# Optimization experiments

Hardware: AMD Instinct MI355X
Metric: run time of the kernel (lower is better)

The kernel has to match this reference:

```python
import jax, jax.numpy as jnp
import numpy as np

B, S, D, H = 4, 2048, 1024, 16
HD = D // H


def setup_inputs() -> dict:
    key = jax.random.key(0)
    ks = jax.random.split(key, 5)
    s_in = 1.0 / np.sqrt(D)
    return {
        "x": jax.random.normal(ks[0], (B, S, D), dtype=jnp.float32),
        "W_attn": jax.random.uniform(ks[1], (D, 3 * D), dtype=jnp.float32, minval=-s_in, maxval=s_in),
        "b_attn": jax.random.uniform(ks[2], (3 * D,), dtype=jnp.float32, minval=-s_in, maxval=s_in),
        "W_proj": jax.random.uniform(ks[3], (D, D), dtype=jnp.float32, minval=-s_in, maxval=s_in),
        "b_proj": jax.random.uniform(ks[4], (D,), dtype=jnp.float32, minval=-s_in, maxval=s_in),
    }


def reference(x, W_attn, b_attn, W_proj, b_proj):
    b, s, d = x.shape
    qkv = x @ W_attn + b_attn                      # [B,S,3D]
    q, k, v = jnp.split(qkv, 3, axis=-1)
    # [B,H,S,HD]
    q = q.reshape(b, s, H, HD).transpose(0, 2, 1, 3)
    k = k.reshape(b, s, H, HD).transpose(0, 2, 1, 3)
    v = v.reshape(b, s, H, HD).transpose(0, 2, 1, 3)
    scale = 1.0 / np.sqrt(HD)
    att = jnp.einsum("bhqd,bhkd->bhqk", q, k) * scale
    causal = jnp.tril(jnp.ones((s, s), dtype=bool))
    att = jnp.where(causal[None, None], att, -jnp.inf)
    att = jax.nn.softmax(att, axis=-1)
    y = jnp.einsum("bhqk,bhkd->bhqd", att, v)      # [B,H,S,HD]
    y = y.transpose(0, 2, 1, 3).reshape(b, s, d)
    return y @ W_proj + b_proj
```

## Files before the change

### kernel.cpp

```cpp
#include <hip/hip_runtime.h>

#define B_  4
#define S_  2048
#define D_  1024
#define H_  16
#define HD_ 64
#define BS_ (B_*S_)

typedef _Float16 f16;
typedef _Float16 f16_8 __attribute__((ext_vector_type(8)));
typedef float    f32_4 __attribute__((ext_vector_type(4)));
typedef unsigned int u32;

#define MFMA16(a,b,c) __builtin_amdgcn_mfma_f32_16x16x32_f16(a, b, c, 0, 0, 0)
#define NEG_INF (-__builtin_inff())

__device__ inline void gl_lds16(const f16* g, f16* lds_base, int chunk_base) {
    __builtin_amdgcn_global_load_lds(
        (const __attribute__((address_space(1))) u32*)g,
        (__attribute__((address_space(3))) u32*)(lds_base + (size_t)chunk_base * 8),
        16, 0, 0);
}

__global__ __launch_bounds__(256) void trans_w(
    const float* __restrict__ W, f16* __restrict__ Wt, int ncols)
{
    __shared__ f16 T[64][72];
    const int t = threadIdx.x;
    const int n0 = blockIdx.x * 64, k0 = blockIdx.y * 64;
    const int nl4 = (t & 15) * 4;
    #pragma unroll
    for (int r = 0; r < 4; r++) {
        const int kl = (t >> 4) + r * 16;
        float4 v = *(const float4*)&W[(size_t)(k0 + kl) * ncols + n0 + nl4];
        T[nl4 + 0][kl] = (f16)v.x;
        T[nl4 + 1][kl] = (f16)v.y;
        T[nl4 + 2][kl] = (f16)v.z;
        T[nl4 + 3][kl] = (f16)v.w;
    }
    __syncthreads();
    const int nr = t >> 2, kc = (t & 3) * 16;
    *(uint4*)&Wt[(size_t)(n0 + nr) * 1024 + k0 + kc]     = *(uint4*)&T[nr][kc];
    *(uint4*)&Wt[(size_t)(n0 + nr) * 1024 + k0 + kc + 8] = *(uint4*)&T[nr][kc + 8];
}

__global__ __launch_bounds__(256) void qkv_gemm(
    const float* __restrict__ X,
    const f16*   __restrict__ Wta,
    const float* __restrict__ bias,
    f16* __restrict__ Qb, f16* __restrict__ Kb, f16* __restrict__ Vt)
{
    __shared__ f16 lds[17408];
    f16* Af = lds;
    f16* Bs = lds + 128*40;
    f16* Ct = lds;

    const int t    = threadIdx.x;
    const int lane = t & 63;
    const int w    = t >> 6;
    const int quad = lane >> 4, l15 = lane & 15;
    const int wr = w >> 1, wc = w & 1;
    const int n0 = blockIdx.x * 128;
    const int m0 = blockIdx.y * 128;

    f32_4 acc[4][4] = {};
    const int am = t >> 1, ak = (t & 1) * 16;
    const int wbase = t & 192;

    for (int k0 = 0; k0 < 1024; k0 += 32) {
        #pragma unroll
        for (int c = 0; c < 2; c++) {
            int i = c*256 + t;
            gl_lds16(Wta + (size_t)(n0 + (i >> 2)) * 1024 + k0 + (i & 3) * 8,
                     Bs, c*256 + wbase);
        }
        {
            const float* xs = X + (size_t)(m0 + am) * 1024 + k0 + ak;
            float4 a0 = *(const float4*)(xs);
            float4 a1 = *(const float4*)(xs + 4);
            float4 a2 = *(const float4*)(xs + 8);
            float4 a3 = *(const float4*)(xs + 12);
            f16 hb[16] = {(f16)a0.x,(f16)a0.y,(f16)a0.z,(f16)a0.w,
                          (f16)a1.x,(f16)a1.y,(f16)a1.z,(f16)a1.w,
                          (f16)a2.x,(f16)a2.y,(f16)a2.z,(f16)a2.w,
                          (f16)a3.x,(f16)a3.y,(f16)a3.z,(f16)a3.w};
            *(uint4*)&Af[am*40 + ak]     = *(uint4*)&hb[0];
            *(uint4*)&Af[am*40 + ak + 8] = *(uint4*)&hb[8];
        }
        __syncthreads();

        f16_8 af[4], bf[4];
        #pragma unroll
        for (int mi = 0; mi < 4; mi++)
            af[mi] = *(const f16_8*)&Af[(wr*64 + mi*16 + l15)*40 + quad*8];
        #pragma unroll
        for (int ni = 0; ni < 4; ni++)
            bf[ni] = *(const f16_8*)&Bs[(wc*64 + ni*16 + l15)*32 + quad*8];
        #pragma unroll
        for (int mi = 0; mi < 4; mi++)
            #pragma unroll
            for (int ni = 0; ni < 4; ni++)
                acc[mi][ni] = MFMA16(af[mi], bf[ni], acc[mi][ni]);
        __syncthreads();
    }

    const int which = n0 >> 10;
    float bcol[4];
    #pragma unroll
    for (int ni = 0; ni < 4; ni++)
        bcol[ni] = bias[n0 + wc*64 + ni*16 + l15];

    if (which < 2) {
        f16* dst = (which == 0) ? Qb : Kb;
        const float sc = (which == 0) ? 0.125f * 1.44269504f : 1.0f;
        #pragma unroll
        for (int mi = 0; mi < 4; mi++)
        #pragma unroll
        for (int ni = 0; ni < 4; ni++)
        #pragma unroll
        for (int r = 0; r < 4; r++) {
            int m = m0 + wr*64 + mi*16 + quad*4 + r;
            int n = (n0 & 1023) + wc*64 + ni*16 + l15;
            int h = n >> 6, hd = n & 63;
            int b = m >> 11, s = m & 2047;
            dst[((size_t)(b*16 + h)*2048 + s)*64 + hd] =
                (f16)((acc[mi][ni][r] + bcol[ni]) * sc);
        }
    } else {
        #pragma unroll
        for (int mi = 0; mi < 4; mi++)
        #pragma unroll
        for (int ni = 0; ni < 4; ni++)
        #pragma unroll
        for (int r = 0; r < 4; r++) {
            int nl = wc*64 + ni*16 + l15;
            int ml = wr*64 + mi*16 + quad*4 + r;
            Ct[nl*136 + ml] = (f16)(acc[mi][ni][r] + bcol[ni]);
        }
        __syncthreads();
        const int row = t >> 1, sc4 = (t & 1) * 64;
        const int n = (n0 & 1023) + row;
        const int h = n >> 6, hd = n & 63;
        const int b = m0 >> 11, s0 = (m0 & 2047) + sc4;
        f16* dst = Vt + ((size_t)(b*16 + h)*64 + hd)*2048 + s0;
        #pragma unroll
        for (int j = 0; j < 8; j++)
            *(uint4*)&dst[j*8] = *(uint4*)&Ct[row*136 + sc4 + j*8];
    }
}

__global__ __launch_bounds__(256) void attn(
    const f16* __restrict__ Qb,
    const f16* __restrict__ Kb,
    const f16* __restrict__ Vt,
    f16* __restrict__ Y)
{
    __shared__ f16 Ks[64*72];
    __shared__ f16 Vs[64*72];
    __shared__ f16 Pl[4][32*72];

    const int t    = threadIdx.x;
    const int w    = t >> 6;
    const int lane = t & 63;
    const int quad = lane >> 4, l15 = lane & 15;
    const int bh   = blockIdx.y;
    const int b    = bh >> 4, h = bh & 15;

    const f16* qh = Qb + (size_t)bh * S_ * 64;
    const f16* kh = Kb + (size_t)bh * S_ * 64;
    const f16* vt = Vt + (size_t)bh * 64 * S_;

    const int sk = t >> 2, sc = (t & 3) * 8;
    const f16_8 ones = {(f16)1,(f16)1,(f16)1,(f16)1,(f16)1,(f16)1,(f16)1,(f16)1};

    #pragma unroll 1
    for (int sp = 0; sp < 2; sp++) {
        const int qb = sp ? 15 - (int)blockIdx.x : (int)blockIdx.x;
        const int qw = qb*128 + w*32;

        f16_8 qa[2][2];
        #pragma unroll
        for (int rt = 0; rt < 2; rt++)
            #pragma unroll
            for (int c = 0; c < 2; c++)
                qa[rt][c] = *(const f16_8*)&qh[(size_t)(qw + rt*16 + l15)*64 + c*32 + quad*8];

        f32_4 o[2][4] = {};
        f32_4 lacc[2] = {};
        const int ntiles = 2*qb + 2;

        for (int kt = 0; kt < ntiles; kt++) {
            const int kbase = kt * 64;
            *(uint4*)&Ks[sk*72 + sc]      = *(const uint4*)&kh[(size_t)(kbase + sk)*64 + sc];
            *(uint4*)&Ks[sk*72 + sc + 32] = *(const uint4*)&kh[(size_t)(kbase + sk)*64 + sc + 32];
            *(uint4*)&Vs[sk*72 + sc]      = *(const uint4*)&vt[(size_t)sk*2048 + kbase + sc];
            *(uint4*)&Vs[sk*72 + sc + 32] = *(const uint4*)&vt[(size_t)sk*2048 + kbase + sc + 32];
            __syncthreads();

            if (kbase <= qw + 31) {
                f16_8 kb[4][2];
                #pragma unroll
                for (int sub = 0; sub < 4; sub++)
                    #pragma unroll
                    for (int c = 0; c < 2; c++)
                        kb[sub][c] = *(const f16_8*)&Ks[(sub*16 + l15)*72 + c*32 + quad*8];
                f32_4 s[2][4];
                #pragma unroll
                for (int rt = 0; rt < 2; rt++)
                    #pragma unroll
                    for (int sub = 0; sub < 4; sub++) {
                        f32_4 a = {};
                        a = MFMA16(qa[rt][0], kb[sub][0], a);
                        a = MFMA16(qa[rt][1], kb[sub][1], a);
                        s[rt][sub] = a;
                    }

                const bool masked = (kbase + 63 > qw);
                #pragma unroll
                for (int rt = 0; rt < 2; rt++)
                #pragma unroll
                for (int r = 0; r < 4; r++) {
                    float v0 = s[rt][0][r], v1 = s[rt][1][r];
                    float v2 = s[rt][2][r], v3 = s[rt][3][r];
                    if (masked) {
                        const int row = qw + rt*16 + quad*4 + r;
                        v0 = (kbase      + l15 <= row) ? v0 : NEG_INF;
                        v1 = (kbase + 16 + l15 <= row) ? v1 : NEG_INF;
                        v2 = (kbase + 32 + l15 <= row) ? v2 : NEG_INF;
                        v3 = (kbase + 48 + l15 <= row) ? v3 : NEG_INF;
                    }
                    const int prow = (rt*16 + quad*4 + r)*72;
                    Pl[w][prow +      l15] = (f16)__builtin_amdgcn_exp2f(v0);
                    Pl[w][prow + 16 + l15] = (f16)__builtin_amdgcn_exp2f(v1);
                    Pl[w][prow + 32 + l15] = (f16)__builtin_amdgcn_exp2f(v2);
                    Pl[w][prow + 48 + l15] = (f16)__builtin_amdgcn_exp2f(v3);
                }
                asm volatile("s_waitcnt lgkmcnt(0)" ::: "memory");

                f16_8 vb[4][2];
                #pragma unroll
                for (int tt = 0; tt < 4; tt++)
                    #pragma unroll
                    for (int c = 0; c < 2; c++)
                        vb[tt][c] = *(const f16_8*)&Vs[(tt*16 + l15)*72 + c*32 + quad*8];
                #pragma unroll
                for (int rt = 0; rt < 2; rt++) {
                    f16_8 pa0 = *(const f16_8*)&Pl[w][(rt*16 + l15)*72 +      quad*8];
                    f16_8 pa1 = *(const f16_8*)&Pl[w][(rt*16 + l15)*72 + 32 + quad*8];
                    lacc[rt] = MFMA16(pa0, ones, lacc[rt]);
                    lacc[rt] = MFMA16(pa1, ones, lacc[rt]);
                    #pragma unroll
                    for (int tt = 0; tt < 4; tt++) {
                        o[rt][tt] = MFMA16(pa0, vb[tt][0], o[rt][tt]);
                        o[rt][tt] = MFMA16(pa1, vb[tt][1], o[rt][tt]);
                    }
                }
            }
            __syncthreads();
        }

        #pragma unroll
        for (int rt = 0; rt < 2; rt++)
        #pragma unroll
        for (int r = 0; r < 4; r++) {
            float inv = 1.0f / lacc[rt][r];
            int srow = qw + rt*16 + quad*4 + r;
            #pragma unroll
            for (int tt = 0; tt < 4; tt++)
                Y[(size_t)(b*S_ + srow)*1024 + h*64 + tt*16 + l15] =
                    (f16)(o[rt][tt][r] * inv);
        }
    }
}

__global__ __launch_bounds__(256) void proj_gemm(
    const f16* __restrict__ Yb,
    const f16* __restrict__ Wtp,
    const float* __restrict__ bias,
    float* __restrict__ Out)
{
    __shared__ f16 lds2[128*32*2];
    f16* Af = lds2;
    f16* Bs = lds2 + 128*32;

    const int t    = threadIdx.x;
    const int lane = t & 63;
    const int w    = t >> 6;
    const int quad = lane >> 4, l15 = lane & 15;
    const int wr = w >> 1, wc = w & 1;
    const int n0 = blockIdx.x * 128;
    const int m0 = blockIdx.y * 128;
    const int wbase = t & 192;

    f32_4 acc[4][4] = {};

    for (int k0 = 0; k0 < 1024; k0 += 32) {
        #pragma unroll
        for (int c = 0; c < 2; c++) {
            int i = c*256 + t;
            gl_lds16(Yb  + (size_t)(m0 + (i >> 2)) * 1024 + k0 + (i & 3) * 8, Af, c*256 + wbase);
            gl_lds16(Wtp + (size_t)(n0 + (i >> 2)) * 1024 + k0 + (i & 3) * 8, Bs, c*256 + wbase);
        }
        __syncthreads();
        f16_8 af[4], bf[4];
        #pragma unroll
        for (int mi = 0; mi < 4; mi++)
            af[mi] = *(const f16_8*)&Af[(wr*64 + mi*16 + l15)*32 + quad*8];
        #pragma unroll
        for (int ni = 0; ni < 4; ni++)
            bf[ni] = *(const f16_8*)&Bs[(wc*64 + ni*16 + l15)*32 + quad*8];
        #pragma unroll
        for (int mi = 0; mi < 4; mi++)
            #pragma unroll
            for (int ni = 0; ni < 4; ni++)
                acc[mi][ni] = MFMA16(af[mi], bf[ni], acc[mi][ni]);
        __syncthreads();
    }

    #pragma unroll
    for (int mi = 0; mi < 4; mi++)
    #pragma unroll
    for (int ni = 0; ni < 4; ni++)
    #pragma unroll
    for (int r = 0; r < 4; r++) {
        int m = m0 + wr*64 + mi*16 + quad*4 + r;
        int n = n0 + wc*64 + ni*16 + l15;
        Out[(size_t)m*1024 + n] = acc[mi][ni][r] + bias[n];
    }
}

extern "C" void kernel_launch(void* const* d_in, const int* in_sizes, int n_in,
                              void* d_out, int out_size, void* d_ws, size_t ws_size,
                              hipStream_t stream) {
    const float* x      = (const float*)d_in[0];
    const float* W_attn = (const float*)d_in[1];
    const float* b_attn = (const float*)d_in[2];
    const float* W_proj = (const float*)d_in[3];
    const float* b_proj = (const float*)d_in[4];
    float* out = (float*)d_out;

    const size_t per = (size_t)B_ * H_ * S_ * HD_;
    f16* Yb  = (f16*)d_ws;
    f16* Wta = Yb;
    f16* Qb  = Yb + per;
    f16* Kb  = Qb + per;
    f16* Vt  = Kb + per;
    f16* Wtp = Qb;

    trans_w  <<<dim3(48, 16), 256, 0, stream>>>(W_attn, Wta, 3*D_);
    qkv_gemm <<<dim3(24, 64), 256, 0, stream>>>(x, Wta, b_attn, Qb, Kb, Vt);
    attn     <<<dim3(8, 64),  256, 0, stream>>>(Qb, Kb, Vt, Yb);
    trans_w  <<<dim3(16, 16), 256, 0, stream>>>(W_proj, Wtp, D_);
    proj_gemm<<<dim3(8, 64),  256, 0, stream>>>(Yb, Wtp, b_proj, out);
}
```

Measured before the change: 301.1 us.

## Keep attention probabilities in registers, pre-convert X to fp16, widen GEMM K-step

Attention now computes S transposed (K as the A operand), so each lane's exp'd scores already form the A fragment of a 16x16x16 MFMA for the PV product. This removes the per-wave LDS round trip for P and its waitcnt. A separate x2h kernel converts X to fp16 in the output buffer, which lets qkv_gemm load A with direct global-to-LDS loads. Both GEMMs stage 64 K per barrier pair instead of 32. In exchange there is an extra kernel launch and an extra pass over X, and the PV product uses smaller MFMAs (twice as many instructions).

```diff
diff --git a/kernel.cpp b/kernel.cpp
--- a/kernel.cpp
+++ b/kernel.cpp
@@ -9,10 +9,12 @@
 
 typedef _Float16 f16;
 typedef _Float16 f16_8 __attribute__((ext_vector_type(8)));
+typedef _Float16 f16_4 __attribute__((ext_vector_type(4)));
 typedef float    f32_4 __attribute__((ext_vector_type(4)));
 typedef unsigned int u32;
 
-#define MFMA16(a,b,c) __builtin_amdgcn_mfma_f32_16x16x32_f16(a, b, c, 0, 0, 0)
+#define MFMA32(a,b,c) __builtin_amdgcn_mfma_f32_16x16x32_f16(a, b, c, 0, 0, 0)
+#define MFMA16(a,b,c) __builtin_amdgcn_mfma_f32_16x16x16f16(a, b, c, 0, 0, 0)
 #define NEG_INF (-__builtin_inff())
 
 __device__ inline void gl_lds16(const f16* g, f16* lds_base, int chunk_base) {
@@ -20,6 +22,17 @@
         (const __attribute__((address_space(1))) u32*)g,
         (__attribute__((address_space(3))) u32*)(lds_base + (size_t)chunk_base * 8),
         16, 0, 0);
+}
+
+__global__ __launch_bounds__(256) void x2h(
+    const float* __restrict__ X, f16* __restrict__ Xh)
+{
+    const size_t i = ((size_t)blockIdx.x * 256 + threadIdx.x) * 8;
+    float4 a = *(const float4*)&X[i];
+    float4 b = *(const float4*)&X[i + 4];
+    f16 h[8] = {(f16)a.x,(f16)a.y,(f16)a.z,(f16)a.w,
+                (f16)b.x,(f16)b.y,(f16)b.z,(f16)b.w};
+    *(uint4*)&Xh[i] = *(const uint4*)h;
 }
 
 __global__ __launch_bounds__(256) void trans_w(
@@ -45,243 +58,15 @@
 }
 
 __global__ __launch_bounds__(256) void qkv_gemm(
-    const float* __restrict__ X,
+    const f16*   __restrict__ Xh,
     const f16*   __restrict__ Wta,
     const float* __restrict__ bias,
     f16* __restrict__ Qb, f16* __restrict__ Kb, f16* __restrict__ Vt)
 {
     __shared__ f16 lds[17408];
-    f16* Af = lds;
-    f16* Bs = lds + 128*40;
-    f16* Ct = lds;
-
-    const int t    = threadIdx.x;
-    const int lane = t & 63;
-    const int w    = t >> 6;
-    const int quad = lane >> 4, l15 = lane & 15;
-    const int wr = w >> 1, wc = w & 1;
-    const int n0 = blockIdx.x * 128;
-    const int m0 = blockIdx.y * 128;
-
-    f32_4 acc[4][4] = {};
-    const int am = t >> 1, ak = (t & 1) * 16;
-    const int wbase = t & 192;
-
-    for (int k0 = 0; k0 < 1024; k0 += 32) {
-        #pragma unroll
-        for (int c = 0; c < 2; c++) {
-            int i = c*256 + t;
-            gl_lds16(Wta + (size_t)(n0 + (i >> 2)) * 1024 + k0 + (i & 3) * 8,
-                     Bs, c*256 + wbase);
-        }
-        {
-            const float* xs = X + (size_t)(m0 + am) * 1024 + k0 + ak;
-            float4 a0 = *(const float4*)(xs);
-            float4 a1 = *(const float4*)(xs + 4);
-            float4 a2 = *(const float4*)(xs + 8);
-            float4 a3 = *(const float4*)(xs + 12);
-            f16 hb[16] = {(f16)a0.x,(f16)a0.y,(f16)a0.z,(f16)a0.w,
-                          (f16)a1.x,(f16)a1.y,(f16)a1.z,(f16)a1.w,
-                          (f16)a2.x,(f16)a2.y,(f16)a2.z,(f16)a2.w,
-                          (f16)a3.x,(f16)a3.y,(f16)a3.z,(f16)a3.w};
-            *(uint4*)&Af[am*40 + ak]     = *(uint4*)&hb[0];
-            *(uint4*)&Af[am*40 + ak + 8] = *(uint4*)&hb[8];
-        }
-        __syncthreads();
-
-        f16_8 af[4], bf[4];
-        #pragma unroll
-        for (int mi = 0; mi < 4; mi++)
-            af[mi] = *(const f16_8*)&Af[(wr*64 + mi*16 + l15)*40 + quad*8];
-        #pragma unroll
-        for (int ni = 0; ni < 4; ni++)
-            bf[ni] = *(const f16_8*)&Bs[(wc*64 + ni*16 + l15)*32 + quad*8];
-        #pragma unroll
-        for (int mi = 0; mi < 4; mi++)
-            #pragma unroll
-            for (int ni = 0; ni < 4; ni++)
-                acc[mi][ni] = MFMA16(af[mi], bf[ni], acc[mi][ni]);
-        __syncthreads();
-    }
-
-    const int which = n0 >> 10;
-    float bcol[4];
-    #pragma unroll
-    for (int ni = 0; ni < 4; ni++)
-        bcol[ni] = bias[n0 + wc*64 + ni*16 + l15];
-
-    if (which < 2) {
-        f16* dst = (which == 0) ? Qb : Kb;
-        const float sc = (which == 0) ? 0.125f * 1.44269504f : 1.0f;
-        #pragma unroll
-        for (int mi = 0; mi < 4; mi++)
-        #pragma unroll
-        for (int ni = 0; ni < 4; ni++)
-        #pragma unroll
-        for (int r = 0; r < 4; r++) {
-            int m = m0 + wr*64 + mi*16 + quad*4 + r;
-            int n = (n0 & 1023) + wc*64 + ni*16 + l15;
-            int h = n >> 6, hd = n & 63;
-            int b = m >> 11, s = m & 2047;
-            dst[((size_t)(b*16 + h)*2048 + s)*64 + hd] =
-                (f16)((acc[mi][ni][r] + bcol[ni]) * sc);
-        }
-    } else {
-        #pragma unroll
-        for (int mi = 0; mi < 4; mi++)
-        #pragma unroll
-        for (int ni = 0; ni < 4; ni++)
-        #pragma unroll
-        for (int r = 0; r < 4; r++) {
-            int nl = wc*64 + ni*16 + l15;
-            int ml = wr*64 + mi*16 + quad*4 + r;
-            Ct[nl*136 + ml] = (f16)(acc[mi][ni][r] + bcol[ni]);
-        }
-        __syncthreads();
-        const int row = t >> 1, sc4 = (t & 1) * 64;
-        const int n = (n0 & 1023) + row;
-        const int h = n >> 6, hd = n & 63;
-        const int b = m0 >> 11, s0 = (m0 & 2047) + sc4;
-        f16* dst = Vt + ((size_t)(b*16 + h)*64 + hd)*2048 + s0;
-        #pragma unroll
-        for (int j = 0; j < 8; j++)
-            *(uint4*)&dst[j*8] = *(uint4*)&Ct[row*136 + sc4 + j*8];
-    }
-}
-
-__global__ __launch_bounds__(256) void attn(
-    const f16* __restrict__ Qb,
-    const f16* __restrict__ Kb,
-    const f16* __restrict__ Vt,
-    f16* __restrict__ Y)
-{
-    __shared__ f16 Ks[64*72];
-    __shared__ f16 Vs[64*72];
-    __shared__ f16 Pl[4][32*72];
-
-    const int t    = threadIdx.x;
-    const int w    = t >> 6;
-    const int lane = t & 63;
-    const int quad = lane >> 4, l15 = lane & 15;
-    const int bh   = blockIdx.y;
-    const int b    = bh >> 4, h = bh & 15;
-
-    const f16* qh = Qb + (size_t)bh * S_ * 64;
-    const f16* kh = Kb + (size_t)bh * S_ * 64;
-    const f16* vt = Vt + (size_t)bh * 64 * S_;
-
-    const int sk = t >> 2, sc = (t & 3) * 8;
-    const f16_8 ones = {(f16)1,(f16)1,(f16)1,(f16)1,(f16)1,(f16)1,(f16)1,(f16)1};
-
-    #pragma unroll 1
-    for (int sp = 0; sp < 2; sp++) {
-        const int qb = sp ? 15 - (int)blockIdx.x : (int)blockIdx.x;
-        const int qw = qb*128 + w*32;
-
-        f16_8 qa[2][2];
-        #pragma unroll
-        for (int rt = 0; rt < 2; rt++)
-            #pragma unroll
-            for (int c = 0; c < 2; c++)
-                qa[rt][c] = *(const f16_8*)&qh[(size_t)(qw + rt*16 + l15)*64 + c*32 + quad*8];
-
-        f32_4 o[2][4] = {};
-        f32_4 lacc[2] = {};
-        const int ntiles = 2*qb + 2;
-
-        for (int kt = 0; kt < ntiles; kt++) {
-            const int kbase = kt * 64;
-            *(uint4*)&Ks[sk*72 + sc]      = *(const uint4*)&kh[(size_t)(kbase + sk)*64 + sc];
-            *(uint4*)&Ks[sk*72 + sc + 32] = *(const uint4*)&kh[(size_t)(kbase + sk)*64 + sc + 32];
-            *(uint4*)&Vs[sk*72 + sc]      = *(const uint4*)&vt[(size_t)sk*2048 + kbase + sc];
-            *(uint4*)&Vs[sk*72 + sc + 32] = *(const uint4*)&vt[(size_t)sk*2048 + kbase + sc + 32];
-            __syncthreads();
-
-            if (kbase <= qw + 31) {
-                f16_8 kb[4][2];
-                #pragma unroll
-                for (int sub = 0; sub < 4; sub++)
-                    #pragma unroll
-                    for (int c = 0; c < 2; c++)
-                        kb[sub][c] = *(const f16_8*)&Ks[(sub*16 + l15)*72 + c*32 + quad*8];
-                f32_4 s[2][4];
-                #pragma unroll
-                for (int rt = 0; rt < 2; rt++)
-                    #pragma unroll
-                    for (int sub = 0; sub < 4; sub++) {
-                        f32_4 a = {};
-                        a = MFMA16(qa[rt][0], kb[sub][0], a);
-                        a = MFMA16(qa[rt][1], kb[sub][1], a);
-                        s[rt][sub] = a;
-                    }
-
-                const bool masked = (kbase + 63 > qw);
-                #pragma unroll
-                for (int rt = 0; rt < 2; rt++)
-                #pragma unroll
-                for (int r = 0; r < 4; r++) {
-                    float v0 = s[rt][0][r], v1 = s[rt][1][r];
-                    float v2 = s[rt][2][r], v3 = s[rt][3][r];
-                    if (masked) {
-                        const int row = qw + rt*16 + quad*4 + r;
-                        v0 = (kbase      + l15 <= row) ? v0 : NEG_INF;
-                        v1 = (kbase + 16 + l15 <= row) ? v1 : NEG_INF;
-                        v2 = (kbase + 32 + l15 <= row) ? v2 : NEG_INF;
-                        v3 = (kbase + 48 + l15 <= row) ? v3 : NEG_INF;
-                    }
-                    const int prow = (rt*16 + quad*4 + r)*72;
-                    Pl[w][prow +      l15] = (f16)__builtin_amdgcn_exp2f(v0);
-                    Pl[w][prow + 16 + l15] = (f16)__builtin_amdgcn_exp2f(v1);
-                    Pl[w][prow + 32 + l15] = (f16)__builtin_amdgcn_exp2f(v2);
-                    Pl[w][prow + 48 + l15] = (f16)__builtin_amdgcn_exp2f(v3);
-                }
-                asm volatile("s_waitcnt lgkmcnt(0)" ::: "memory");
-
-                f16_8 vb[4][2];
-                #pragma unroll
-                for (int tt = 0; tt < 4; tt++)
-                    #pragma unroll
-                    for (int c = 0; c < 2; c++)
-                        vb[tt][c] = *(const f16_8*)&Vs[(tt*16 + l15)*72 + c*32 + quad*8];
-                #pragma unroll
-                for (int rt = 0; rt < 2; rt++) {
-                    f16_8 pa0 = *(const f16_8*)&Pl[w][(rt*16 + l15)*72 +      quad*8];
-                    f16_8 pa1 = *(const f16_8*)&Pl[w][(rt*16 + l15)*72 + 32 + quad*8];
-                    lacc[rt] = MFMA16(pa0, ones, lacc[rt]);
-                    lacc[rt] = MFMA16(pa1, ones, lacc[rt]);
-                    #pragma unroll
-                    for (int tt = 0; tt < 4; tt++) {
-                        o[rt][tt] = MFMA16(pa0, vb[tt][0], o[rt][tt]);
-                        o[rt][tt] = MFMA16(pa1, vb[tt][1], o[rt][tt]);
-                    }
-                }
-            }
-            __syncthreads();
-        }
-
-        #pragma unroll
-        for (int rt = 0; rt < 2; rt++)
-        #pragma unroll
-        for (int r = 0; r < 4; r++) {
-            float inv = 1.0f / lacc[rt][r];
-            int srow = qw + rt*16 + quad*4 + r;
-            #pragma unroll
-            for (int tt = 0; tt < 4; tt++)
-                Y[(size_t)(b*S_ + srow)*1024 + h*64 + tt*16 + l15] =
-                    (f16)(o[rt][tt][r] * inv);
-        }
-    }
-}
-
-__global__ __launch_bounds__(256) void proj_gemm(
-    const f16* __restrict__ Yb,
-    const f16* __restrict__ Wtp,
-    const float* __restrict__ bias,
-    float* __restrict__ Out)
-{
-    __shared__ f16 lds2[128*32*2];
-    f16* Af = lds2;
-    f16* Bs = lds2 + 128*32;
+    f16* Af[2] = {lds,        lds + 4096};
+    f16* Bf[2] = {lds + 8192, lds + 12288};
+    f16* Ct    = lds;
 
     const int t    = threadIdx.x;
     const int lane = t & 63;
@@ -294,26 +79,249 @@
 
     f32_4 acc[4][4] = {};
 
-    for (int k0 = 0; k0 < 1024; k0 += 32) {
-        #pragma unroll
-        for (int c = 0; c < 2; c++) {
-            int i = c*256 + t;
-            gl_lds16(Yb  + (size_t)(m0 + (i >> 2)) * 1024 + k0 + (i & 3) * 8, Af, c*256 + wbase);
-            gl_lds16(Wtp + (size_t)(n0 + (i >> 2)) * 1024 + k0 + (i & 3) * 8, Bs, c*256 + wbase);
-        }
-        __syncthreads();
-        f16_8 af[4], bf[4];
+    for (int k0 = 0; k0 < 1024; k0 += 64) {
+        #pragma unroll
+        for (int kc = 0; kc < 2; kc++)
+            #pragma unroll
+            for (int c = 0; c < 2; c++) {
+                int i = c*256 + t;
+                const int row = i >> 2, col = (i & 3) * 8;
+                gl_lds16(Xh  + (size_t)(m0 + row)*1024 + k0 + kc*32 + col,
+                         Af[kc], c*256 + wbase);
+                gl_lds16(Wta + (size_t)(n0 + row)*1024 + k0 + kc*32 + col,
+                         Bf[kc], c*256 + wbase);
+            }
+        __syncthreads();
+
+        #pragma unroll
+        for (int kc = 0; kc < 2; kc++) {
+            f16_8 af[4], bf[4];
+            #pragma unroll
+            for (int mi = 0; mi < 4; mi++)
+                af[mi] = *(const f16_8*)&Af[kc][(wr*64 + mi*16 + l15)*32 + quad*8];
+            #pragma unroll
+            for (int ni = 0; ni < 4; ni++)
+                bf[ni] = *(const f16_8*)&Bf[kc][(wc*64 + ni*16 + l15)*32 + quad*8];
+            #pragma unroll
+            for (int mi = 0; mi < 4; mi++)
+                #pragma unroll
+                for (int ni = 0; ni < 4; ni++)
+                    acc[mi][ni] = MFMA32(af[mi], bf[ni], acc[mi][ni]);
+        }
+        __syncthreads();
+    }
+
+    const int which = n0 >> 10;
+    float bcol[4];
+    #pragma unroll
+    for (int ni = 0; ni < 4; ni++)
+        bcol[ni] = bias[n0 + wc*64 + ni*16 + l15];
+
+    if (which < 2) {
+        f16* dst = (which == 0) ? Qb : Kb;
+        const float sc = (which == 0) ? 0.125f * 1.44269504f : 1.0f;
         #pragma unroll
         for (int mi = 0; mi < 4; mi++)
-            af[mi] = *(const f16_8*)&Af[(wr*64 + mi*16 + l15)*32 + quad*8];
         #pragma unroll
         for (int ni = 0; ni < 4; ni++)
-            bf[ni] = *(const f16_8*)&Bs[(wc*64 + ni*16 + l15)*32 + quad*8];
+        #pragma unroll
+        for (int r = 0; r < 4; r++) {
+            int m = m0 + wr*64 + mi*16 + quad*4 + r;
+            int n = (n0 & 1023) + wc*64 + ni*16 + l15;
+            int h = n >> 6, hd = n & 63;
+            int b = m >> 11, s = m & 2047;
+            dst[((size_t)(b*16 + h)*2048 + s)*64 + hd] =
+                (f16)((acc[mi][ni][r] + bcol[ni]) * sc);
+        }
+    } else {
         #pragma unroll
         for (int mi = 0; mi < 4; mi++)
+        #pragma unroll
+        for (int ni = 0; ni < 4; ni++)
+        #pragma unroll
+        for (int r = 0; r < 4; r++) {
+            int nl = wc*64 + ni*16 + l15;
+            int ml = wr*64 + mi*16 + quad*4 + r;
+            Ct[nl*136 + ml] = (f16)(acc[mi][ni][r] + bcol[ni]);
+        }
+        __syncthreads();
+        const int row = t >> 1, sc4 = (t & 1) * 64;
+        const int n = (n0 & 1023) + row;
+        const int h = n >> 6, hd = n & 63;
+        const int b = m0 >> 11, s0 = (m0 & 2047) + sc4;
+        f16* dst = Vt + ((size_t)(b*16 + h)*64 + hd)*2048 + s0;
+        #pragma unroll
+        for (int j = 0; j < 8; j++)
+            *(uint4*)&dst[j*8] = *(uint4*)&Ct[row*136 + sc4 + j*8];
+    }
+}
+
+__global__ __launch_bounds__(256) void attn(
+    const f16* __restrict__ Qb,
+    const f16* __restrict__ Kb,
+    const f16* __restrict__ Vt,
+    f16* __restrict__ Y)
+{
+    __shared__ f16 Ks[64*72];
+    __shared__ f16 Vs[64*72];
+
+    const int t    = threadIdx.x;
+    const int w    = t >> 6;
+    const int lane = t & 63;
+    const int quad = lane >> 4, l15 = lane & 15;
+    const int bh   = blockIdx.y;
+    const int b    = bh >> 4, h = bh & 15;
+
+    const f16* qh = Qb + (size_t)bh * S_ * 64;
+    const f16* kh = Kb + (size_t)bh * S_ * 64;
+    const f16* vt = Vt + (size_t)bh * 64 * S_;
+
+    const int sk = t >> 2, sc = (t & 3) * 8;
+    const f16_4 ones = {(f16)1,(f16)1,(f16)1,(f16)1};
+
+    #pragma unroll 1
+    for (int sp = 0; sp < 2; sp++) {
+        const int qb = sp ? 15 - (int)blockIdx.x : (int)blockIdx.x;
+        const int qw = qb*128 + w*32;
+
+        f16_8 qa[2][2];
+        #pragma unroll
+        for (int rt = 0; rt < 2; rt++)
+            #pragma unroll
+            for (int c = 0; c < 2; c++)
+                qa[rt][c] = *(const f16_8*)&qh[(size_t)(qw + rt*16 + l15)*64 + c*32 + quad*8];
+
+        f32_4 o[2][4] = {};
+        f32_4 lacc[2] = {};
+        const int ntiles = 2*qb + 2;
+
+        for (int kt = 0; kt < ntiles; kt++) {
+            const int kbase = kt * 64;
+            *(uint4*)&Ks[sk*72 + sc]      = *(const uint4*)&kh[(size_t)(kbase + sk)*64 + sc];
+            *(uint4*)&Ks[sk*72 + sc + 32] = *(const uint4*)&kh[(size_t)(kbase + sk)*64 + sc + 32];
+            *(uint4*)&Vs[sk*72 + sc]      = *(const uint4*)&vt[(size_t)sk*2048 + kbase + sc];
+            *(uint4*)&Vs[sk*72 + sc + 32] = *(const uint4*)&vt[(size_t)sk*2048 + kbase + sc + 32];
+            __syncthreads();
+
+            if (kbase <= qw + 31) {
+                f16_8 kb[4][2];
+                #pragma unroll
+                for (int sub = 0; sub < 4; sub++)
+                    #pragma unroll
+                    for (int c = 0; c < 2; c++)
+                        kb[sub][c] = *(const f16_8*)&Ks[(sub*16 + l15)*72 + c*32 + quad*8];
+                f32_4 st[2][4];
+                #pragma unroll
+                for (int rt = 0; rt < 2; rt++)
+                    #pragma unroll
+                    for (int sub = 0; sub < 4; sub++) {
+                        f32_4 a = {};
+                        a = MFMA32(kb[sub][0], qa[rt][0], a);
+                        a = MFMA32(kb[sub][1], qa[rt][1], a);
+                        st[rt][sub] = a;
+                    }
+
+                const bool masked = (kbase + 63 > qw);
+                f16_4 pt[2][4];
+                #pragma unroll
+                for (int rt = 0; rt < 2; rt++)
+                #pragma unroll
+                for (int sub = 0; sub < 4; sub++) {
+                    const int qrow = qw + rt*16 + l15;
+                    f16_4 p;
+                    #pragma unroll
+                    for (int r = 0; r < 4; r++) {
+                        float v = st[rt][sub][r];
+                        if (masked) {
+                            int key = kbase + sub*16 + quad*4 + r;
+                            v = (key <= qrow) ? v : NEG_INF;
+                        }
+                        p[r] = (f16)__builtin_amdgcn_exp2f(v);
+                    }
+                    pt[rt][sub] = p;
+                }
+
+                #pragma unroll
+                for (int sub = 0; sub < 4; sub++) {
+                    f16_4 vb[4];
+                    #pragma unroll
+                    for (int tt = 0; tt < 4; tt++)
+                        vb[tt] = *(const f16_4*)&Vs[(tt*16 + l15)*72 + sub*16 + quad*4];
+                    #pragma unroll
+                    for (int rt = 0; rt < 2; rt++) {
+                        lacc[rt] = MFMA16(pt[rt][sub], ones, lacc[rt]);
+                        #pragma unroll
+                        for (int tt = 0; tt < 4; tt++)
+                            o[rt][tt] = MFMA16(pt[rt][sub], vb[tt], o[rt][tt]);
+                    }
+                }
+            }
+            __syncthreads();
+        }
+
+        #pragma unroll
+        for (int rt = 0; rt < 2; rt++)
+        #pragma unroll
+        for (int r = 0; r < 4; r++) {
+            float inv = 1.0f / lacc[rt][r];
+            int srow = qw + rt*16 + quad*4 + r;
+            #pragma unroll
+            for (int tt = 0; tt < 4; tt++)
+                Y[(size_t)(b*S_ + srow)*1024 + h*64 + tt*16 + l15] =
+                    (f16)(o[rt][tt][r] * inv);
+        }
+    }
+}
+
+__global__ __launch_bounds__(256) void proj_gemm(
+    const f16* __restrict__ Yb,
+    const f16* __restrict__ Wtp,
+    const float* __restrict__ bias,
+    float* __restrict__ Out)
+{
+    __shared__ f16 lds2[16384];
+    f16* Af[2] = {lds2,        lds2 + 4096};
+    f16* Bf[2] = {lds2 + 8192, lds2 + 12288};
+
+    const int t    = threadIdx.x;
+    const int lane = t & 63;
+    const int w    = t >> 6;
+    const int quad = lane >> 4, l15 = lane & 15;
+    const int wr = w >> 1, wc = w & 1;
+    const int n0 = blockIdx.x * 128;
+    const int m0 = blockIdx.y * 128;
+    const int wbase = t & 192;
+
+    f32_4 acc[4][4] = {};
+
+    for (int k0 = 0; k0 < 1024; k0 += 64) {
+        #pragma unroll
+        for (int kc = 0; kc < 2; kc++)
+            #pragma unroll
+            for (int c = 0; c < 2; c++) {
+                int i = c*256 + t;
+                const int row = i >> 2, col = (i & 3) * 8;
+                gl_lds16(Yb  + (size_t)(m0 + row)*1024 + k0 + kc*32 + col,
+                         Af[kc], c*256 + wbase);
+                gl_lds16(Wtp + (size_t)(n0 + row)*1024 + k0 + kc*32 + col,
+                         Bf[kc], c*256 + wbase);
+            }
+        __syncthreads();
+        #pragma unroll
+        for (int kc = 0; kc < 2; kc++) {
+            f16_8 af[4], bf[4];
+            #pragma unroll
+            for (int mi = 0; mi < 4; mi++)
+                af[mi] = *(const f16_8*)&Af[kc][(wr*64 + mi*16 + l15)*32 + quad*8];
             #pragma unroll
             for (int ni = 0; ni < 4; ni++)
-                acc[mi][ni] = MFMA16(af[mi], bf[ni], acc[mi][ni]);
+                bf[ni] = *(const f16_8*)&Bf[kc][(wc*64 + ni*16 + l15)*32 + quad*8];
+            #pragma unroll
+            for (int mi = 0; mi < 4; mi++)
+                #pragma unroll
+                for (int ni = 0; ni < 4; ni++)
+                    acc[mi][ni] = MFMA32(af[mi], bf[ni], acc[mi][ni]);
+        }
         __syncthreads();
     }
 
@@ -346,9 +354,11 @@
     f16* Kb  = Qb + per;
     f16* Vt  = Kb + per;
     f16* Wtp = Qb;
-
+    f16* Xh  = (f16*)d_out;
+
+    x2h      <<<BS_*D_/(256*8), 256, 0, stream>>>(x, Xh);
     trans_w  <<<dim3(48, 16), 256, 0, stream>>>(W_attn, Wta, 3*D_);
-    qkv_gemm <<<dim3(24, 64), 256, 0, stream>>>(x, Wta, b_attn, Qb, Kb, Vt);
+    qkv_gemm <<<dim3(24, 64), 256, 0, stream>>>(Xh, Wta, b_attn, Qb, Kb, Vt);
     attn     <<<dim3(8, 64),  256, 0, stream>>>(Qb, Kb, Vt, Yb);
     trans_w  <<<dim3(16, 16), 256, 0, stream>>>(W_proj, Wtp, D_);
     proj_gemm<<<dim3(8, 64),  256, 0, stream>>>(Yb, Wtp, b_proj, out);
```

New measurement: 284.8 us. 1.06x faster.
